# Performance work log

Measured on AMD Instinct MI355X. Metric: run time of the kernel, lower is better.

Reference implementation:

```python
import jax, jax.numpy as jnp
import numpy as np

N_NODES = 100000
N_EDGES = 800000
NUM_FEATURES = 81
NUM_BOND = 22
OUT_CHANNEL = 64
D_COORD = 3  # 'distance' rule applies to feature indices [0:3]


def setup_inputs() -> dict:
    key = jax.random.key(0)
    k1, k2, k3, k4, k5, k6 = jax.random.split(key, 6)
    features = jax.random.normal(k1, (N_NODES, NUM_FEATURES), dtype=jnp.float32)
    bond = jax.random.normal(k2, (N_EDGES, NUM_BOND), dtype=jnp.float32)
    w_s = jax.random.normal(k3, (NUM_FEATURES, OUT_CHANNEL), dtype=jnp.float32) * 0.1
    w_n = jax.random.normal(k4, (NUM_FEATURES + NUM_BOND, OUT_CHANNEL), dtype=jnp.float32) * 0.1
    src = jax.random.randint(k5, (N_EDGES,), 0, N_NODES)
    dst = jax.random.randint(k6, (N_EDGES,), 0, N_NODES)
    return {"features": features, "bond": bond, "w_s": w_s, "w_n": w_n,
            "src": src, "dst": dst}


def reference(features, bond, w_s, w_n, src, dst):
    # Gather endpoint features per edge: [E, F]
    self_f = features[src]
    nbr_f = features[dst]

    # Rule 1: 'distance' on [0:3] -> keep neighbour coords, compute L2 distance
    diff = self_f[:, :D_COORD] - nbr_f[:, :D_COORD]
    dist = jnp.sqrt(jnp.sum(diff * diff, axis=-1))      # [E]
    d = jnp.where(dist > 0, dist, jnp.float32(0.01))

    # Rule 2 (last, single-index): 'sum' on [3:]
    seg1 = nbr_f[:, :D_COORD]                           # [E, 3]
    seg2 = self_f[:, D_COORD:] + nbr_f[:, D_COORD:]     # [E, 78]

    # Distance normalization applies to the whole combined vector (pre-bond)
    combined = jnp.concatenate([seg1, seg2], axis=-1) / (d * d)[:, None]
    edge_vec = jnp.concatenate([combined, bond], axis=-1)  # [E, F + B]

    contrib = edge_vec @ w_n                            # [E, out]
    agg = jax.ops.segment_sum(contrib, src, num_segments=features.shape[0])
    return features @ w_s + agg                         # [N, out]
```

## Files before the change

kernel.cpp:

```cpp
#include <hip/hip_runtime.h>

#define N_NODES 100000
#define N_EDGES 800000
#define NF 81
#define NB 22
#define OC 64
#define SCAN_CHUNK 1024
#define SCAN_BLOCKS ((N_NODES + SCAN_CHUNK - 1) / SCAN_CHUNK)
#define ASTRIDE 68

__global__ __launch_bounds__(256) void k_node3(
    const float* __restrict__ feat, const float* __restrict__ w_s,
    const float* __restrict__ w_n, float* __restrict__ out,
    float* __restrict__ pb, float4* __restrict__ xyz)
{
    __shared__ float shA[NF * ASTRIDE];
    __shared__ float shW[NF * 128];
    const int t  = threadIdx.x;
    const int n0 = blockIdx.x * 64;

    for (int idx = t; idx < NF * OC; idx += 256) {
        const int k = idx >> 6, c = idx & 63;
        shW[k * 128 + c]      = w_s[idx];
        shW[k * 128 + 64 + c] = w_n[idx];
    }
    const long gbase = (long)n0 * NF;
    for (int f = t; f < 64 * NF; f += 256) {
        const int n = f / NF;
        const int k = f - n * NF;
        const float v = (gbase + f < (long)N_NODES * NF) ? feat[gbase + f] : 0.f;
        shA[k * ASTRIDE + n] = v;
    }
    __syncthreads();

    if (t < 64 && n0 + t < N_NODES)
        xyz[n0 + t] = make_float4(shA[0 * ASTRIDE + t], shA[1 * ASTRIDE + t],
                                  shA[2 * ASTRIDE + t], 0.f);

    const int tx = t & 15;
    const int ty = t >> 4;
    float acc[32];
#pragma unroll
    for (int q = 0; q < 32; ++q) acc[q] = 0.f;

    const float* ap = shA + tx * 4;
    const float* wp = shW + ty * 8;
#pragma unroll 3
    for (int k = 0; k < NF; ++k) {
        const float4 a  = *(const float4*)(ap + k * ASTRIDE);
        const float4 w0 = *(const float4*)(wp + k * 128);
        const float4 w1 = *(const float4*)(wp + k * 128 + 4);
        const float av[4] = {a.x, a.y, a.z, a.w};
        const float wv[8] = {w0.x, w0.y, w0.z, w0.w, w1.x, w1.y, w1.z, w1.w};
#pragma unroll
        for (int i = 0; i < 4; ++i)
#pragma unroll
            for (int j = 0; j < 8; ++j)
                acc[i * 8 + j] += av[i] * wv[j];
    }

    float* dbase = (ty < 8) ? out : pb;
    const int cb = (ty & 7) * 8;
#pragma unroll
    for (int i = 0; i < 4; ++i) {
        const int node = n0 + tx * 4 + i;
        if (node < N_NODES) {
            float* p = dbase + (long)node * OC + cb;
            *(float4*)(p)     = make_float4(acc[i*8+0], acc[i*8+1], acc[i*8+2], acc[i*8+3]);
            *(float4*)(p + 4) = make_float4(acc[i*8+4], acc[i*8+5], acc[i*8+6], acc[i*8+7]);
        }
    }
}

__global__ void k_hist(const int* __restrict__ src, int* __restrict__ cnt) {
    const int e = blockIdx.x * blockDim.x + threadIdx.x;
    if (e < N_EDGES) atomicAdd(&cnt[src[e]], 1);
}

__global__ __launch_bounds__(256) void k_scan_blk(
    const int* __restrict__ cnt, int* __restrict__ row, int* __restrict__ bsum)
{
    __shared__ int sh[256];
    const int t = threadIdx.x;
    const int base = blockIdx.x * SCAN_CHUNK + t * 4;
    int c0 = 0, c1 = 0, c2 = 0, c3 = 0;
    if (base + 3 < N_NODES) {
        const int4 c = *(const int4*)(cnt + base);
        c0 = c.x; c1 = c.y; c2 = c.z; c3 = c.w;
    } else {
        if (base + 0 < N_NODES) c0 = cnt[base + 0];
        if (base + 1 < N_NODES) c1 = cnt[base + 1];
        if (base + 2 < N_NODES) c2 = cnt[base + 2];
    }
    const int s = c0 + c1 + c2 + c3;
    sh[t] = s;
    __syncthreads();
    for (int off = 1; off < 256; off <<= 1) {
        int v = sh[t];
        int a = (t >= off) ? sh[t - off] : 0;
        __syncthreads();
        sh[t] = v + a;
        __syncthreads();
    }
    const int excl = sh[t] - s;
    if (t == 255) bsum[blockIdx.x] = sh[255];
    if (base + 3 < N_NODES) {
        int4 r;
        r.x = excl; r.y = excl + c0; r.z = excl + c0 + c1; r.w = excl + c0 + c1 + c2;
        *(int4*)(row + base) = r;
    } else {
        int e = excl;
        if (base + 0 < N_NODES) { row[base + 0] = e; e += c0; }
        if (base + 1 < N_NODES) { row[base + 1] = e; e += c1; }
        if (base + 2 < N_NODES) { row[base + 2] = e; }
    }
}

__global__ void k_scan_top(int* __restrict__ bsum, int* __restrict__ row) {
    __shared__ int sh[128];
    const int t = threadIdx.x;
    const int v = (t < SCAN_BLOCKS) ? bsum[t] : 0;
    sh[t] = v;
    __syncthreads();
    for (int off = 1; off < 128; off <<= 1) {
        int x = sh[t];
        int a = (t >= off) ? sh[t - off] : 0;
        __syncthreads();
        sh[t] = x + a;
        __syncthreads();
    }
    if (t < SCAN_BLOCKS) bsum[t] = sh[t] - v;
    if (t == 127) row[N_NODES] = sh[127];
}

__global__ __launch_bounds__(256) void k_scan_add(
    int* __restrict__ row, int* __restrict__ cursor, const int* __restrict__ bsum)
{
    const int off = bsum[blockIdx.x];
    const int base = blockIdx.x * SCAN_CHUNK + threadIdx.x * 4;
    if (base + 3 < N_NODES) {
        int4 r = *(const int4*)(row + base);
        r.x += off; r.y += off; r.z += off; r.w += off;
        *(int4*)(row + base) = r;
        *(int4*)(cursor + base) = r;
    } else {
#pragma unroll
        for (int k = 0; k < 4; ++k)
            if (base + k < N_NODES) {
                const int v = row[base + k] + off;
                row[base + k] = v;
                cursor[base + k] = v;
            }
    }
}

__device__ inline unsigned pk_bf16(float a, float b) {
    const unsigned ua = (__float_as_uint(a) + 0x8000u) >> 16;
    const unsigned ub = (__float_as_uint(b) + 0x8000u) & 0xffff0000u;
    return ua | ub;
}

__global__ void k_prep(const int* __restrict__ src, const int* __restrict__ dst,
                       const float* __restrict__ bond, const float4* __restrict__ xyz,
                       int* __restrict__ cursor, unsigned* __restrict__ rec)
{
    const int e = blockIdx.x * blockDim.x + threadIdx.x;
    if (e >= N_EDGES) return;
    const int s = src[e];
    const int d = dst[e];
    const float4 a = xyz[s], b = xyz[d];
    const float dx = a.x - b.x, dy = a.y - b.y, dz = a.z - b.z;
    const float d2 = dx * dx + dy * dy + dz * dz;
    const float inv = (d2 > 0.f) ? __builtin_amdgcn_rcpf(d2) : 1.0e4f;

    float bv[NB];
    const float2* bp = (const float2*)(bond + (long)e * NB);
#pragma unroll
    for (int j = 0; j < NB / 2; ++j) {
        const float2 v = bp[j];
        bv[2 * j] = v.x; bv[2 * j + 1] = v.y;
    }

    unsigned p[11];
#pragma unroll
    for (int j = 0; j < 11; ++j) p[j] = pk_bf16(bv[2 * j], bv[2 * j + 1]);

    const int pos = atomicAdd(&cursor[s], 1);
    unsigned* r = rec + (size_t)pos * 16;
    *(uint4*)(r)     = make_uint4(p[0], p[1], p[2], p[3]);
    *(uint4*)(r + 4) = make_uint4(p[4], p[5], p[6], p[7]);
    *(uint4*)(r + 8) = make_uint4(p[8], p[9], p[10], __float_as_uint(inv));
    *(uint2*)(r + 12) = make_uint2((unsigned)d, 0u);
}

__global__ __launch_bounds__(256) void k_gather(
    const int* __restrict__ row, const unsigned* __restrict__ rec,
    const float* __restrict__ w_n, const float* __restrict__ pb,
    const float4* __restrict__ xyz, float* __restrict__ out)
{
    const int lane = threadIdx.x & 63;
    const int wid  = (int)((blockIdx.x * blockDim.x + threadIdx.x) >> 6);
    if (wid >= N_NODES) return;
    const int n = __builtin_amdgcn_readfirstlane(wid);

    float wnb[NB];
#pragma unroll
    for (int j = 0; j < NB; ++j) wnb[j] = w_n[(NF + j) * OC + lane];
    const float w0 = w_n[0 * OC + lane];
    const float w1 = w_n[1 * OC + lane];
    const float w2 = w_n[2 * OC + lane];

    const int rs = row[n], re = row[n + 1];
    const float4 xs = xyz[n];
    const float pa = pb[(long)n * OC + lane]
                   - (xs.x * w0 + xs.y * w1 + xs.z * w2);

    float acc = 0.f;
    int i = rs;
    for (; i + 2 <= re; i += 2) {
        const unsigned* rA = rec + (size_t)i * 16;
        const unsigned* rB = rA + 16;
        unsigned pA[13], pB[13];
#pragma unroll
        for (int j = 0; j < 13; ++j) pA[j] = rA[j];
#pragma unroll
        for (int j = 0; j < 13; ++j) pB[j] = rB[j];
        const float invA = __uint_as_float(pA[11]);
        const float invB = __uint_as_float(pB[11]);
        const int   tA   = (int)pA[12];
        const int   tB   = (int)pB[12];
        const float pbtA = pb[(long)tA * OC + lane];
        const float pbtB = pb[(long)tB * OC + lane];

        float cA = invA * (pa + pbtA);
        float cB = invB * (pa + pbtB);
#pragma unroll
        for (int j = 0; j < 11; ++j) {
            cA += __uint_as_float(pA[j] << 16)        * wnb[2 * j]
                + __uint_as_float(pA[j] & 0xffff0000u) * wnb[2 * j + 1];
            cB += __uint_as_float(pB[j] << 16)        * wnb[2 * j]
                + __uint_as_float(pB[j] & 0xffff0000u) * wnb[2 * j + 1];
        }
        acc += cA + cB;
    }
    if (i < re) {
        const unsigned* r = rec + (size_t)i * 16;
        unsigned p[13];
#pragma unroll
        for (int j = 0; j < 13; ++j) p[j] = r[j];
        const float inv = __uint_as_float(p[11]);
        const int   tt  = (int)p[12];
        const float pbt = pb[(long)tt * OC + lane];
        float c = inv * (pa + pbt);
#pragma unroll
        for (int j = 0; j < 11; ++j)
            c += __uint_as_float(p[j] << 16)        * wnb[2 * j]
               + __uint_as_float(p[j] & 0xffff0000u) * wnb[2 * j + 1];
        acc += c;
    }

    out[(long)n * OC + lane] += acc;
}

extern "C" void kernel_launch(void* const* d_in, const int* in_sizes, int n_in,
                              void* d_out, int out_size, void* d_ws, size_t ws_size,
                              hipStream_t stream) {
    const float* feat = (const float*)d_in[0];
    const float* bond = (const float*)d_in[1];
    const float* w_s  = (const float*)d_in[2];
    const float* w_n  = (const float*)d_in[3];
    const int*   src  = (const int*)d_in[4];
    const int*   dstv = (const int*)d_in[5];
    float* out = (float*)d_out;

    char* base = (char*)d_ws;
    float*    pb     = (float*)   (base);
    float4*   xyz    = (float4*)  (base + 25600000);
    int*      row    = (int*)     (base + 27200000);
    int*      cnt    = (int*)     (base + 27600016);
    int*      cursor = (int*)     (base + 28000016);
    int*      bsum   = (int*)     (base + 28400016);
    unsigned* rec    = (unsigned*)(base + 28400576);

    hipMemsetAsync(cnt, 0, N_NODES * sizeof(int), stream);

    k_node3   <<<(N_NODES + 63) / 64, 256, 0, stream>>>(feat, w_s, w_n, out, pb, xyz);
    k_hist    <<<(N_EDGES + 255) / 256, 256, 0, stream>>>(src, cnt);
    k_scan_blk<<<SCAN_BLOCKS, 256, 0, stream>>>(cnt, row, bsum);
    k_scan_top<<<1, 128, 0, stream>>>(bsum, row);
    k_scan_add<<<SCAN_BLOCKS, 256, 0, stream>>>(row, cursor, bsum);
    k_prep    <<<(N_EDGES + 255) / 256, 256, 0, stream>>>(src, dstv, bond, xyz,
                                                          cursor, rec);
    k_gather  <<<(N_NODES * 64 + 255) / 256, 256, 0, stream>>>(row, rec, w_n, pb,
                                                               xyz, out);
}
```

Baseline: 378.0 us.

## Store neighbor projection in bf16, widen edge records, factor bond matmul out of edge loop

The node kernel now reads weights straight from global memory with register prefetch instead of staging them in shared memory, uses a node-major feature tile, and writes the neighbor projection table as bf16, halving its size. Edge records grow to 32 dwords holding fp32 bond values plus inv and dst, so per-edge bf16 packing disappears from prep. The gather kernel sums bond vectors and inverse distances per node and applies the bond weights and self projection once after the loop. Per-edge work drops to a few adds, at the cost of more record traffic and bf16 rounding of the projected features.

```diff
diff --git a/kernel.cpp b/kernel.cpp
--- a/kernel.cpp
+++ b/kernel.cpp
@@ -7,67 +7,89 @@
 #define OC 64
 #define SCAN_CHUNK 1024
 #define SCAN_BLOCKS ((N_NODES + SCAN_CHUNK - 1) / SCAN_CHUNK)
-#define ASTRIDE 68
-
-__global__ __launch_bounds__(256) void k_node3(
+#define AS 84
+#define REC_DW 32
+
+typedef __attribute__((ext_vector_type(2))) float v2f;
+
+__device__ inline unsigned pk2bf16(float a, float b) {
+    const unsigned ua = (__float_as_uint(a) + 0x8000u) >> 16;
+    const unsigned ub = (__float_as_uint(b) + 0x8000u) & 0xffff0000u;
+    return ua | ub;
+}
+__device__ inline float bf2f(unsigned u) { return __uint_as_float(u << 16); }
+
+__global__ __launch_bounds__(256) void k_node4(
     const float* __restrict__ feat, const float* __restrict__ w_s,
     const float* __restrict__ w_n, float* __restrict__ out,
-    float* __restrict__ pb, float4* __restrict__ xyz)
-{
-    __shared__ float shA[NF * ASTRIDE];
-    __shared__ float shW[NF * 128];
+    unsigned short* __restrict__ pbh, float4* __restrict__ xyz)
+{
+    __shared__ float shA[64 * AS];
     const int t  = threadIdx.x;
     const int n0 = blockIdx.x * 64;
 
-    for (int idx = t; idx < NF * OC; idx += 256) {
-        const int k = idx >> 6, c = idx & 63;
-        shW[k * 128 + c]      = w_s[idx];
-        shW[k * 128 + 64 + c] = w_n[idx];
-    }
     const long gbase = (long)n0 * NF;
+    const long gtot  = (long)N_NODES * NF;
     for (int f = t; f < 64 * NF; f += 256) {
         const int n = f / NF;
         const int k = f - n * NF;
-        const float v = (gbase + f < (long)N_NODES * NF) ? feat[gbase + f] : 0.f;
-        shA[k * ASTRIDE + n] = v;
+        shA[n * AS + k] = (gbase + f < gtot) ? feat[gbase + f] : 0.f;
     }
     __syncthreads();
 
     if (t < 64 && n0 + t < N_NODES)
-        xyz[n0 + t] = make_float4(shA[0 * ASTRIDE + t], shA[1 * ASTRIDE + t],
-                                  shA[2 * ASTRIDE + t], 0.f);
+        xyz[n0 + t] = make_float4(shA[t * AS + 0], shA[t * AS + 1],
+                                  shA[t * AS + 2], 0.f);
 
     const int tx = t & 15;
     const int ty = t >> 4;
-    float acc[32];
-#pragma unroll
-    for (int q = 0; q < 32; ++q) acc[q] = 0.f;
-
-    const float* ap = shA + tx * 4;
-    const float* wp = shW + ty * 8;
+    const float* W = ((ty < 8) ? w_s : w_n) + (ty & 7) * 8;
+
+    float acc[4][8];
+#pragma unroll
+    for (int i = 0; i < 4; ++i)
+#pragma unroll
+        for (int j = 0; j < 8; ++j) acc[i][j] = 0.f;
+
+    const float* a0p = shA + (tx * 4 + 0) * AS;
+    const float* a1p = shA + (tx * 4 + 1) * AS;
+    const float* a2p = shA + (tx * 4 + 2) * AS;
+    const float* a3p = shA + (tx * 4 + 3) * AS;
+
+    float4 wc0 = *(const float4*)(W);
+    float4 wc1 = *(const float4*)(W + 4);
 #pragma unroll 3
     for (int k = 0; k < NF; ++k) {
-        const float4 a  = *(const float4*)(ap + k * ASTRIDE);
-        const float4 w0 = *(const float4*)(wp + k * 128);
-        const float4 w1 = *(const float4*)(wp + k * 128 + 4);
-        const float av[4] = {a.x, a.y, a.z, a.w};
-        const float wv[8] = {w0.x, w0.y, w0.z, w0.w, w1.x, w1.y, w1.z, w1.w};
+        const int kn = (k + 1 < NF) ? k + 1 : k;
+        const float4 wn0 = *(const float4*)(W + kn * OC);
+        const float4 wn1 = *(const float4*)(W + kn * OC + 4);
+        const float a0 = a0p[k], a1 = a1p[k], a2 = a2p[k], a3 = a3p[k];
+        const float av[4] = {a0, a1, a2, a3};
+        const float wv[8] = {wc0.x, wc0.y, wc0.z, wc0.w,
+                             wc1.x, wc1.y, wc1.z, wc1.w};
 #pragma unroll
         for (int i = 0; i < 4; ++i)
 #pragma unroll
             for (int j = 0; j < 8; ++j)
-                acc[i * 8 + j] += av[i] * wv[j];
-    }
-
-    float* dbase = (ty < 8) ? out : pb;
+                acc[i][j] += av[i] * wv[j];
+        wc0 = wn0; wc1 = wn1;
+    }
+
     const int cb = (ty & 7) * 8;
 #pragma unroll
     for (int i = 0; i < 4; ++i) {
         const int node = n0 + tx * 4 + i;
-        if (node < N_NODES) {
-            float* p = dbase + (long)node * OC + cb;
-            *(float4*)(p)     = make_float4(acc[i*8+0], acc[i*8+1], acc[i*8+2], acc[i*8+3]);
-            *(float4*)(p + 4) = make_float4(acc[i*8+4], acc[i*8+5], acc[i*8+6], acc[i*8+7]);
+        if (node >= N_NODES) continue;
+        if (ty < 8) {
+            float* p = out + (long)node * OC + cb;
+            *(float4*)(p)     = make_float4(acc[i][0], acc[i][1], acc[i][2], acc[i][3]);
+            *(float4*)(p + 4) = make_float4(acc[i][4], acc[i][5], acc[i][6], acc[i][7]);
+        } else {
+            unsigned* p = (unsigned*)(pbh + (long)node * OC + cb);
+            *(uint4*)p = make_uint4(pk2bf16(acc[i][0], acc[i][1]),
+                                    pk2bf16(acc[i][2], acc[i][3]),
+                                    pk2bf16(acc[i][4], acc[i][5]),
+                                    pk2bf16(acc[i][6], acc[i][7]));
         }
     }
 }
@@ -154,12 +176,6 @@
     }
 }
 
-__device__ inline unsigned pk_bf16(float a, float b) {
-    const unsigned ua = (__float_as_uint(a) + 0x8000u) >> 16;
-    const unsigned ub = (__float_as_uint(b) + 0x8000u) & 0xffff0000u;
-    return ua | ub;
-}
-
 __global__ void k_prep(const int* __restrict__ src, const int* __restrict__ dst,
                        const float* __restrict__ bond, const float4* __restrict__ xyz,
                        int* __restrict__ cursor, unsigned* __restrict__ rec)
@@ -181,21 +197,20 @@
         bv[2 * j] = v.x; bv[2 * j + 1] = v.y;
     }
 
-    unsigned p[11];
-#pragma unroll
-    for (int j = 0; j < 11; ++j) p[j] = pk_bf16(bv[2 * j], bv[2 * j + 1]);
-
     const int pos = atomicAdd(&cursor[s], 1);
-    unsigned* r = rec + (size_t)pos * 16;
-    *(uint4*)(r)     = make_uint4(p[0], p[1], p[2], p[3]);
-    *(uint4*)(r + 4) = make_uint4(p[4], p[5], p[6], p[7]);
-    *(uint4*)(r + 8) = make_uint4(p[8], p[9], p[10], __float_as_uint(inv));
-    *(uint2*)(r + 12) = make_uint2((unsigned)d, 0u);
+    unsigned* r = rec + (size_t)pos * REC_DW;
+    *(uint4*)(r + 0)  = make_uint4(__float_as_uint(inv), (unsigned)d,
+                                   __float_as_uint(bv[0]), __float_as_uint(bv[1]));
+#pragma unroll
+    for (int q = 0; q < 5; ++q)
+        *(uint4*)(r + 4 + q * 4) = make_uint4(
+            __float_as_uint(bv[2 + 4 * q + 0]), __float_as_uint(bv[2 + 4 * q + 1]),
+            __float_as_uint(bv[2 + 4 * q + 2]), __float_as_uint(bv[2 + 4 * q + 3]));
 }
 
 __global__ __launch_bounds__(256) void k_gather(
     const int* __restrict__ row, const unsigned* __restrict__ rec,
-    const float* __restrict__ w_n, const float* __restrict__ pb,
+    const float* __restrict__ w_n, const unsigned short* __restrict__ pbh,
     const float4* __restrict__ xyz, float* __restrict__ out)
 {
     const int lane = threadIdx.x & 63;
@@ -212,54 +227,60 @@
 
     const int rs = row[n], re = row[n + 1];
     const float4 xs = xyz[n];
-    const float pa = pb[(long)n * OC + lane]
+    const float pa = bf2f(pbh[(long)n * OC + lane])
                    - (xs.x * w0 + xs.y * w1 + xs.z * w2);
 
-    float acc = 0.f;
+    float acc = 0.f, sinv = 0.f;
+    v2f bsum[11];
+#pragma unroll
+    for (int j = 0; j < 11; ++j) bsum[j] = (v2f){0.f, 0.f};
+
     int i = rs;
     for (; i + 2 <= re; i += 2) {
-        const unsigned* rA = rec + (size_t)i * 16;
-        const unsigned* rB = rA + 16;
-        unsigned pA[13], pB[13];
-#pragma unroll
-        for (int j = 0; j < 13; ++j) pA[j] = rA[j];
-#pragma unroll
-        for (int j = 0; j < 13; ++j) pB[j] = rB[j];
-        const float invA = __uint_as_float(pA[11]);
-        const float invB = __uint_as_float(pB[11]);
-        const int   tA   = (int)pA[12];
-        const int   tB   = (int)pB[12];
-        const float pbtA = pb[(long)tA * OC + lane];
-        const float pbtB = pb[(long)tB * OC + lane];
-
-        float cA = invA * (pa + pbtA);
-        float cB = invB * (pa + pbtB);
+        const unsigned* rA = rec + (size_t)i * REC_DW;
+        const unsigned* rB = rA + REC_DW;
+        unsigned a[24], b[24];
+#pragma unroll
+        for (int j = 0; j < 24; ++j) a[j] = rA[j];
+#pragma unroll
+        for (int j = 0; j < 24; ++j) b[j] = rB[j];
+        const float invA = __uint_as_float(a[0]);
+        const float invB = __uint_as_float(b[0]);
+        const int   tA   = (int)a[1];
+        const int   tB   = (int)b[1];
+        const float pbtA = bf2f(pbh[(long)tA * OC + lane]);
+        const float pbtB = bf2f(pbh[(long)tB * OC + lane]);
+        acc  += invA * pbtA + invB * pbtB;
+        sinv += invA + invB;
 #pragma unroll
         for (int j = 0; j < 11; ++j) {
-            cA += __uint_as_float(pA[j] << 16)        * wnb[2 * j]
-                + __uint_as_float(pA[j] & 0xffff0000u) * wnb[2 * j + 1];
-            cB += __uint_as_float(pB[j] << 16)        * wnb[2 * j]
-                + __uint_as_float(pB[j] & 0xffff0000u) * wnb[2 * j + 1];
+            const v2f va = {__uint_as_float(a[2 + 2 * j]), __uint_as_float(a[3 + 2 * j])};
+            const v2f vb = {__uint_as_float(b[2 + 2 * j]), __uint_as_float(b[3 + 2 * j])};
+            bsum[j] += va + vb;
         }
-        acc += cA + cB;
     }
     if (i < re) {
-        const unsigned* r = rec + (size_t)i * 16;
-        unsigned p[13];
-#pragma unroll
-        for (int j = 0; j < 13; ++j) p[j] = r[j];
-        const float inv = __uint_as_float(p[11]);
-        const int   tt  = (int)p[12];
-        const float pbt = pb[(long)tt * OC + lane];
-        float c = inv * (pa + pbt);
-#pragma unroll
-        for (int j = 0; j < 11; ++j)
-            c += __uint_as_float(p[j] << 16)        * wnb[2 * j]
-               + __uint_as_float(p[j] & 0xffff0000u) * wnb[2 * j + 1];
-        acc += c;
-    }
-
-    out[(long)n * OC + lane] += acc;
+        const unsigned* rA = rec + (size_t)i * REC_DW;
+        unsigned a[24];
+#pragma unroll
+        for (int j = 0; j < 24; ++j) a[j] = rA[j];
+        const float invA = __uint_as_float(a[0]);
+        const int   tA   = (int)a[1];
+        acc  += invA * bf2f(pbh[(long)tA * OC + lane]);
+        sinv += invA;
+#pragma unroll
+        for (int j = 0; j < 11; ++j) {
+            const v2f va = {__uint_as_float(a[2 + 2 * j]), __uint_as_float(a[3 + 2 * j])};
+            bsum[j] += va;
+        }
+    }
+
+    float bacc = 0.f;
+#pragma unroll
+    for (int j = 0; j < 11; ++j)
+        bacc += bsum[j].x * wnb[2 * j] + bsum[j].y * wnb[2 * j + 1];
+
+    out[(long)n * OC + lane] += acc + pa * sinv + bacc;
 }
 
 extern "C" void kernel_launch(void* const* d_in, const int* in_sizes, int n_in,
@@ -274,23 +295,23 @@
     float* out = (float*)d_out;
 
     char* base = (char*)d_ws;
-    float*    pb     = (float*)   (base);
-    float4*   xyz    = (float4*)  (base + 25600000);
-    int*      row    = (int*)     (base + 27200000);
-    int*      cnt    = (int*)     (base + 27600016);
-    int*      cursor = (int*)     (base + 28000016);
-    int*      bsum   = (int*)     (base + 28400016);
-    unsigned* rec    = (unsigned*)(base + 28400576);
+    float4*         xyz    = (float4*)        (base);
+    unsigned short* pbh    = (unsigned short*)(base + 1600000);
+    int*            row    = (int*)           (base + 14400000);
+    int*            cnt    = (int*)           (base + 14800016);
+    int*            cursor = (int*)           (base + 15200016);
+    int*            bsum   = (int*)           (base + 15600016);
+    unsigned*       rec    = (unsigned*)      (base + 15600640);
 
     hipMemsetAsync(cnt, 0, N_NODES * sizeof(int), stream);
 
-    k_node3   <<<(N_NODES + 63) / 64, 256, 0, stream>>>(feat, w_s, w_n, out, pb, xyz);
+    k_node4   <<<(N_NODES + 63) / 64, 256, 0, stream>>>(feat, w_s, w_n, out, pbh, xyz);
     k_hist    <<<(N_EDGES + 255) / 256, 256, 0, stream>>>(src, cnt);
     k_scan_blk<<<SCAN_BLOCKS, 256, 0, stream>>>(cnt, row, bsum);
     k_scan_top<<<1, 128, 0, stream>>>(bsum, row);
     k_scan_add<<<SCAN_BLOCKS, 256, 0, stream>>>(row, cursor, bsum);
     k_prep    <<<(N_EDGES + 255) / 256, 256, 0, stream>>>(src, dstv, bond, xyz,
                                                           cursor, rec);
-    k_gather  <<<(N_NODES * 64 + 255) / 256, 256, 0, stream>>>(row, rec, w_n, pb,
+    k_gather  <<<(N_NODES * 64 + 255) / 256, 256, 0, stream>>>(row, rec, w_n, pbh,
                                                                xyz, out);
 }
```

Measured after the change: 409.3 us. 8.3% more time.
